# Performance work log

Measured on AMD Instinct MI355X. Metric: run time of the kernel, lower is better.

Reference implementation:

```python
import jax, jax.numpy as jnp
import numpy as np

B = 32768          # batch size (positions)
PIECES = 32        # max active features per position
NNZ = B * PIECES
FT_OUT = 512
NFEAT = 768        # 64 squares * 6 piece types * 2 colors


def setup_inputs() -> dict:
    key = jax.random.key(0)
    k1, k2, k3, k4, k5, k6 = jax.random.split(key, 6)
    rows = jnp.repeat(jnp.arange(B, dtype=jnp.int64), PIECES)  # batch index per nnz
    stm_cols = jax.random.randint(k1, (NNZ,), 0, NFEAT, dtype=jnp.int64)
    nstm_cols = jax.random.randint(k2, (NNZ,), 0, NFEAT, dtype=jnp.int64)
    stm_indices = jnp.stack([rows, stm_cols], axis=0)   # [2, NNZ]
    nstm_indices = jnp.stack([rows, nstm_cols], axis=0)  # [2, NNZ]
    values = jnp.ones((NNZ,), dtype=jnp.float32)
    ft_w = jax.random.normal(k3, (FT_OUT, NFEAT), dtype=jnp.float32) * 0.05
    ft_b = jax.random.normal(k4, (FT_OUT,), dtype=jnp.float32) * 0.05
    out_w = jax.random.normal(k5, (1, 2 * FT_OUT), dtype=jnp.float32) * 0.05
    out_b = jax.random.normal(k6, (1,), dtype=jnp.float32) * 0.05
    return {
        "stm_indices": stm_indices,
        "nstm_indices": nstm_indices,
        "values": values,
        "size": B,
        "ft_w": ft_w,
        "ft_b": ft_b,
        "out_w": out_w,
        "out_b": out_b,
    }


def reference(stm_indices, nstm_indices, values, size, ft_w, ft_b, out_w, out_b):
    # sparse_coo_tensor(...).to_dense(): scatter-add values into dense [size, 768]
    board_stm = jnp.zeros((size, NFEAT), dtype=values.dtype).at[
        stm_indices[0], stm_indices[1]].add(values)
    board_nstm = jnp.zeros((size, NFEAT), dtype=values.dtype).at[
        nstm_indices[0], nstm_indices[1]].add(values)
    # shared feature transformer Linear(768, ft_out)
    stm_ft = board_stm @ ft_w.T + ft_b    # [B, FT_OUT]
    nstm_ft = board_nstm @ ft_w.T + ft_b  # [B, FT_OUT]
    hidden = jnp.clip(jnp.concatenate([stm_ft, nstm_ft], axis=1), 0.0, 1.0)
    return jax.nn.sigmoid(hidden @ out_w.T + out_b)  # [B, 1]
```

## Files before the change

kernel.cpp:

```cpp
#include <hip/hip_runtime.h>

#define BATCH  32768
#define PIECES 32
#define NNZ    (BATCH * PIECES)
#define FT_OUT 512
#define NFEAT  768
#define WSCALE 400.0f

#define POS_PER_BLOCK 32
#define NTHREADS 512
#define NBLOCKS (BATCH / POS_PER_BLOCK)
#define ROW_PITCH 784
#define SIDE_BYTES (POS_PER_BLOCK * ROW_PITCH)
#define PACC_OFF (2 * SIDE_BYTES)
#define LDS_TOTAL (PACC_OFF + 128)
#define SC_PITCH 33

typedef int v4i  __attribute__((ext_vector_type(4)));
typedef int v16i __attribute__((ext_vector_type(16)));

__global__ __launch_bounds__(256) void pack_w_i8(
    const float* __restrict__ ft_w, unsigned char* __restrict__ bpk)
{
    int gid = blockIdx.x * 256 + threadIdx.x;
    int t   = gid / 1536;
    int rem = gid - t * 1536;
    int s   = rem >> 6;
    int l   = rem & 63;
    int g   = l >> 5, ln = l & 31;
    int n   = t * 32 + ln;
    const float* src = ft_w + n * NFEAT + s * 32 + g * 16;
    unsigned ud[4];
    #pragma unroll
    for (int d = 0; d < 4; ++d) {
        unsigned u = 0;
        #pragma unroll
        for (int b = 0; b < 4; ++b) {
            float q = rintf(src[4 * d + b] * WSCALE);
            q = fminf(fmaxf(q, -127.0f), 127.0f);
            u |= ((unsigned)(int)q & 0xffu) << (8 * b);
        }
        ud[d] = u;
    }
    *(uint4*)(bpk + gid * 16) = make_uint4(ud[0], ud[1], ud[2], ud[3]);
}

__global__ __launch_bounds__(NTHREADS, 4) void nn_mfma(
    const int*   __restrict__ stm_idx,
    const int*   __restrict__ nstm_idx,
    const float* __restrict__ values,
    const unsigned char* __restrict__ bpk,
    const float* __restrict__ ft_b,
    const float* __restrict__ out_w,
    const float* __restrict__ out_b,
    float*       __restrict__ out)
{
    extern __shared__ __align__(16) unsigned char lds[];
    unsigned* ldsw = (unsigned*)lds;
    float*    scf  = (float*)lds;
    float*    pacc = (float*)(lds + PACC_OFF);

    const int tid  = threadIdx.x;
    const int pos0 = blockIdx.x * POS_PER_BLOCK;

    int colv[4], vqv[4];
    #pragma unroll
    for (int it = 0; it < 4; ++it) {
        int i    = tid + it * NTHREADS;
        int side = i >> 10;
        int r    = i & 1023;
        int nnz  = pos0 * PIECES + r;
        colv[it] = side ? nstm_idx[NNZ + nnz] : stm_idx[NNZ + nnz];
        vqv[it]  = (int)rintf(values[nnz]);
    }

    for (int i = tid; i < LDS_TOTAL / 16; i += NTHREADS)
        ((uint4*)lds)[i] = make_uint4(0u, 0u, 0u, 0u);
    __syncthreads();

    #pragma unroll
    for (int it = 0; it < 4; ++it) {
        int i    = tid + it * NTHREADS;
        int side = i >> 10;
        int pos  = (i & 1023) >> 5;
        int dw   = (side * SIDE_BYTES + pos * ROW_PITCH) >> 2;
        atomicAdd(&ldsw[dw + (colv[it] >> 2)],
                  (unsigned)vqv[it] << (8 * (colv[it] & 3)));
    }
    __syncthreads();

    const int lane = tid & 63, wv = tid >> 6;
    const int ln = lane & 31, g = lane >> 5;
    const float inv_s = 1.0f / WSCALE;

    v16i acc[2][2];
    #pragma unroll
    for (int q = 0; q < 2; ++q)
        #pragma unroll
        for (int sd = 0; sd < 2; ++sd)
            #pragma unroll
            for (int e = 0; e < 16; ++e) acc[q][sd][e] = 0;

    const unsigned char* a0p = lds + ln * ROW_PITCH + g * 16;
    const unsigned char* a1p = a0p + SIDE_BYTES;
    const unsigned char* bp0 = bpk + ((wv * 2 + 0) * 24) * 1024 + lane * 16;
    const unsigned char* bp1 = bpk + ((wv * 2 + 1) * 24) * 1024 + lane * 16;

    #pragma unroll 4
    for (int ks = 0; ks < 24; ++ks) {
        uint4 aw0 = *(const uint4*)(a0p + ks * 32);
        uint4 aw1 = *(const uint4*)(a1p + ks * 32);
        uint4 bw0 = *(const uint4*)(bp0 + ks * 1024);
        uint4 bw1 = *(const uint4*)(bp1 + ks * 1024);
        v4i af0 = __builtin_bit_cast(v4i, aw0);
        v4i af1 = __builtin_bit_cast(v4i, aw1);
        v4i bf0 = __builtin_bit_cast(v4i, bw0);
        v4i bf1 = __builtin_bit_cast(v4i, bw1);
        acc[0][0] = __builtin_amdgcn_mfma_i32_32x32x32_i8(af0, bf0, acc[0][0], 0, 0, 0);
        acc[0][1] = __builtin_amdgcn_mfma_i32_32x32x32_i8(af1, bf0, acc[0][1], 0, 0, 0);
        acc[1][0] = __builtin_amdgcn_mfma_i32_32x32x32_i8(af0, bf1, acc[1][0], 0, 0, 0);
        acc[1][1] = __builtin_amdgcn_mfma_i32_32x32x32_i8(af1, bf1, acc[1][1], 0, 0, 0);
    }

    float pp[16];
    #pragma unroll
    for (int r = 0; r < 16; ++r) pp[r] = 0.f;

    #pragma unroll
    for (int q = 0; q < 2; ++q) {
        int   n    = (wv * 2 + q) * 32 + ln;
        float bias = ft_b[n];
        float ow0  = out_w[n];
        float ow1  = out_w[FT_OUT + n];
        #pragma unroll
        for (int r = 0; r < 16; ++r) {
            float h0 = fminf(fmaxf((float)acc[q][0][r] * inv_s + bias, 0.f), 1.f);
            float h1 = fminf(fmaxf((float)acc[q][1][r] * inv_s + bias, 0.f), 1.f);
            pp[r] += h0 * ow0 + h1 * ow1;
        }
    }

    __syncthreads();
    {
        int base = wv * (32 * SC_PITCH) + ln * SC_PITCH;
        #pragma unroll
        for (int r = 0; r < 16; ++r) {
            int m = (r & 3) + 8 * (r >> 2) + 4 * g;
            scf[base + m] = pp[r];
        }
    }
    __syncthreads();
    {
        int m = tid & 31, j = tid >> 5;
        float s = 0.f;
        #pragma unroll
        for (int i = 0; i < 16; ++i) {
            int p   = i * 16 + j;
            int wvp = p >> 5, lnp = p & 31;
            s += scf[wvp * (32 * SC_PITCH) + lnp * SC_PITCH + m];
        }
        atomicAdd(&pacc[m], s);
    }
    __syncthreads();

    if (tid < POS_PER_BLOCK) {
        float p = pacc[tid] + out_b[0];
        out[pos0 + tid] = 1.0f / (1.0f + expf(-p));
    }
}

extern "C" void kernel_launch(void* const* d_in, const int* in_sizes, int n_in,
                              void* d_out, int out_size, void* d_ws, size_t ws_size,
                              hipStream_t stream)
{
    const int*   stm    = (const int*)  d_in[0];
    const int*   nstm   = (const int*)  d_in[1];
    const float* values = (const float*)d_in[2];
    const float* ft_w   = (const float*)d_in[4];
    const float* ft_b   = (const float*)d_in[5];
    const float* out_w  = (const float*)d_in[6];
    const float* out_b  = (const float*)d_in[7];

    unsigned char* bpk = (unsigned char*)d_ws;

    (void)hipFuncSetAttribute((const void*)nn_mfma,
                              hipFuncAttributeMaxDynamicSharedMemorySize,
                              LDS_TOTAL);

    pack_w_i8<<<dim3(96), dim3(256), 0, stream>>>(ft_w, bpk);
    nn_mfma<<<dim3(NBLOCKS), dim3(NTHREADS), LDS_TOTAL, stream>>>(
        stm, nstm, values, bpk, ft_b, out_w, out_b, (float*)d_out);
}
```

Measured before the change: 105.1 us.

## Double positions per block to reuse packed weight fragments across more MFMAs

Each block now handles 64 positions instead of 32, so every weight fragment loaded from global memory feeds four MFMAs instead of two, halving total weight traffic. The epilogue reduction runs in two phases, one per 32-position half, reusing the same scratch area in LDS. In exchange LDS per block roughly doubles, accumulator registers double, occupancy hint drops from 4 to 2 blocks per CU, and the grid has half as many blocks.

```diff
diff --git a/kernel.cpp b/kernel.cpp
--- a/kernel.cpp
+++ b/kernel.cpp
@@ -7,13 +7,13 @@
 #define NFEAT  768
 #define WSCALE 400.0f
 
-#define POS_PER_BLOCK 32
+#define POS_PER_BLOCK 64
 #define NTHREADS 512
 #define NBLOCKS (BATCH / POS_PER_BLOCK)
 #define ROW_PITCH 784
 #define SIDE_BYTES (POS_PER_BLOCK * ROW_PITCH)
 #define PACC_OFF (2 * SIDE_BYTES)
-#define LDS_TOTAL (PACC_OFF + 128)
+#define LDS_TOTAL (PACC_OFF + 256)
 #define SC_PITCH 33
 
 typedef int v4i  __attribute__((ext_vector_type(4)));
@@ -45,7 +45,7 @@
     *(uint4*)(bpk + gid * 16) = make_uint4(ud[0], ud[1], ud[2], ud[3]);
 }
 
-__global__ __launch_bounds__(NTHREADS, 4) void nn_mfma(
+__global__ __launch_bounds__(NTHREADS, 2) void nn_mfma(
     const int*   __restrict__ stm_idx,
     const int*   __restrict__ nstm_idx,
     const float* __restrict__ values,
@@ -63,12 +63,12 @@
     const int tid  = threadIdx.x;
     const int pos0 = blockIdx.x * POS_PER_BLOCK;
 
-    int colv[4], vqv[4];
-    #pragma unroll
-    for (int it = 0; it < 4; ++it) {
+    int colv[8], vqv[8];
+    #pragma unroll
+    for (int it = 0; it < 8; ++it) {
         int i    = tid + it * NTHREADS;
-        int side = i >> 10;
-        int r    = i & 1023;
+        int side = i >> 11;
+        int r    = i & 2047;
         int nnz  = pos0 * PIECES + r;
         colv[it] = side ? nstm_idx[NNZ + nnz] : stm_idx[NNZ + nnz];
         vqv[it]  = (int)rintf(values[nnz]);
@@ -79,10 +79,10 @@
     __syncthreads();
 
     #pragma unroll
-    for (int it = 0; it < 4; ++it) {
+    for (int it = 0; it < 8; ++it) {
         int i    = tid + it * NTHREADS;
-        int side = i >> 10;
-        int pos  = (i & 1023) >> 5;
+        int side = i >> 11;
+        int pos  = (i & 2047) >> 5;
         int dw   = (side * SIDE_BYTES + pos * ROW_PITCH) >> 2;
         atomicAdd(&ldsw[dw + (colv[it] >> 2)],
                   (unsigned)vqv[it] << (8 * (colv[it] & 3)));
@@ -93,75 +93,87 @@
     const int ln = lane & 31, g = lane >> 5;
     const float inv_s = 1.0f / WSCALE;
 
-    v16i acc[2][2];
+    v16i acc[2][4];
     #pragma unroll
     for (int q = 0; q < 2; ++q)
         #pragma unroll
-        for (int sd = 0; sd < 2; ++sd)
+        for (int mt = 0; mt < 4; ++mt)
             #pragma unroll
-            for (int e = 0; e < 16; ++e) acc[q][sd][e] = 0;
-
-    const unsigned char* a0p = lds + ln * ROW_PITCH + g * 16;
-    const unsigned char* a1p = a0p + SIDE_BYTES;
+            for (int e = 0; e < 16; ++e) acc[q][mt][e] = 0;
+
+    const unsigned char* ap[4];
+    #pragma unroll
+    for (int mt = 0; mt < 4; ++mt)
+        ap[mt] = lds + (mt >> 1) * SIDE_BYTES
+               + (((mt & 1) * 32) + ln) * ROW_PITCH + g * 16;
     const unsigned char* bp0 = bpk + ((wv * 2 + 0) * 24) * 1024 + lane * 16;
     const unsigned char* bp1 = bpk + ((wv * 2 + 1) * 24) * 1024 + lane * 16;
 
-    #pragma unroll 4
+    #pragma unroll 2
     for (int ks = 0; ks < 24; ++ks) {
-        uint4 aw0 = *(const uint4*)(a0p + ks * 32);
-        uint4 aw1 = *(const uint4*)(a1p + ks * 32);
         uint4 bw0 = *(const uint4*)(bp0 + ks * 1024);
         uint4 bw1 = *(const uint4*)(bp1 + ks * 1024);
+        uint4 aw0 = *(const uint4*)(ap[0] + ks * 32);
+        uint4 aw1 = *(const uint4*)(ap[1] + ks * 32);
+        uint4 aw2 = *(const uint4*)(ap[2] + ks * 32);
+        uint4 aw3 = *(const uint4*)(ap[3] + ks * 32);
+        v4i bf0 = __builtin_bit_cast(v4i, bw0);
+        v4i bf1 = __builtin_bit_cast(v4i, bw1);
         v4i af0 = __builtin_bit_cast(v4i, aw0);
         v4i af1 = __builtin_bit_cast(v4i, aw1);
-        v4i bf0 = __builtin_bit_cast(v4i, bw0);
-        v4i bf1 = __builtin_bit_cast(v4i, bw1);
+        v4i af2 = __builtin_bit_cast(v4i, aw2);
+        v4i af3 = __builtin_bit_cast(v4i, aw3);
         acc[0][0] = __builtin_amdgcn_mfma_i32_32x32x32_i8(af0, bf0, acc[0][0], 0, 0, 0);
         acc[0][1] = __builtin_amdgcn_mfma_i32_32x32x32_i8(af1, bf0, acc[0][1], 0, 0, 0);
+        acc[0][2] = __builtin_amdgcn_mfma_i32_32x32x32_i8(af2, bf0, acc[0][2], 0, 0, 0);
+        acc[0][3] = __builtin_amdgcn_mfma_i32_32x32x32_i8(af3, bf0, acc[0][3], 0, 0, 0);
         acc[1][0] = __builtin_amdgcn_mfma_i32_32x32x32_i8(af0, bf1, acc[1][0], 0, 0, 0);
         acc[1][1] = __builtin_amdgcn_mfma_i32_32x32x32_i8(af1, bf1, acc[1][1], 0, 0, 0);
-    }
-
-    float pp[16];
-    #pragma unroll
-    for (int r = 0; r < 16; ++r) pp[r] = 0.f;
-
-    #pragma unroll
-    for (int q = 0; q < 2; ++q) {
-        int   n    = (wv * 2 + q) * 32 + ln;
-        float bias = ft_b[n];
-        float ow0  = out_w[n];
-        float ow1  = out_w[FT_OUT + n];
+        acc[1][2] = __builtin_amdgcn_mfma_i32_32x32x32_i8(af2, bf1, acc[1][2], 0, 0, 0);
+        acc[1][3] = __builtin_amdgcn_mfma_i32_32x32x32_i8(af3, bf1, acc[1][3], 0, 0, 0);
+    }
+
+    const int   n0   = (wv * 2 + 0) * 32 + ln;
+    const int   n1   = (wv * 2 + 1) * 32 + ln;
+    const float b0   = ft_b[n0],          b1   = ft_b[n1];
+    const float ow00 = out_w[n0],         ow01 = out_w[n1];
+    const float ow10 = out_w[FT_OUT + n0], ow11 = out_w[FT_OUT + n1];
+
+    __syncthreads();
+
+    #pragma unroll
+    for (int ph = 0; ph < 2; ++ph) {
+        float pp[16];
         #pragma unroll
         for (int r = 0; r < 16; ++r) {
-            float h0 = fminf(fmaxf((float)acc[q][0][r] * inv_s + bias, 0.f), 1.f);
-            float h1 = fminf(fmaxf((float)acc[q][1][r] * inv_s + bias, 0.f), 1.f);
-            pp[r] += h0 * ow0 + h1 * ow1;
-        }
-    }
-
-    __syncthreads();
-    {
-        int base = wv * (32 * SC_PITCH) + ln * SC_PITCH;
-        #pragma unroll
-        for (int r = 0; r < 16; ++r) {
-            int m = (r & 3) + 8 * (r >> 2) + 4 * g;
-            scf[base + m] = pp[r];
-        }
-    }
-    __syncthreads();
-    {
-        int m = tid & 31, j = tid >> 5;
-        float s = 0.f;
-        #pragma unroll
-        for (int i = 0; i < 16; ++i) {
-            int p   = i * 16 + j;
-            int wvp = p >> 5, lnp = p & 31;
-            s += scf[wvp * (32 * SC_PITCH) + lnp * SC_PITCH + m];
-        }
-        atomicAdd(&pacc[m], s);
-    }
-    __syncthreads();
+            float h00 = fminf(fmaxf((float)acc[0][ph][r]     * inv_s + b0, 0.f), 1.f);
+            float h01 = fminf(fmaxf((float)acc[1][ph][r]     * inv_s + b1, 0.f), 1.f);
+            float h10 = fminf(fmaxf((float)acc[0][ph + 2][r] * inv_s + b0, 0.f), 1.f);
+            float h11 = fminf(fmaxf((float)acc[1][ph + 2][r] * inv_s + b1, 0.f), 1.f);
+            pp[r] = h00 * ow00 + h01 * ow01 + h10 * ow10 + h11 * ow11;
+        }
+        {
+            int base = wv * (32 * SC_PITCH) + ln * SC_PITCH;
+            #pragma unroll
+            for (int r = 0; r < 16; ++r) {
+                int m = (r & 3) + 8 * (r >> 2) + 4 * g;
+                scf[base + m] = pp[r];
+            }
+        }
+        __syncthreads();
+        {
+            int m = tid & 31, j = tid >> 5;
+            float s = 0.f;
+            #pragma unroll
+            for (int i = 0; i < 16; ++i) {
+                int p   = i * 16 + j;
+                int wvp = p >> 5, lnp = p & 31;
+                s += scf[wvp * (32 * SC_PITCH) + lnp * SC_PITCH + m];
+            }
+            atomicAdd(&pacc[ph * 32 + m], s);
+        }
+        __syncthreads();
+    }
 
     if (tid < POS_PER_BLOCK) {
         float p = pacc[tid] + out_b[0];
```

New measurement: 106.5 us. Within noise of the previous version (+1.3%).

## Process four position groups per block with double-buffered LDS scatter prefetch

Applied to the files above, without the earlier changes.

Each block now handles four groups of 32 positions instead of one. While the MFMA loop runs on the current group, it loads the next group's sparse indices and scatters them into a second LDS buffer. Bias and output-weight loads are hoisted out of the loop, and the occupancy hint drops from 4 to 2 blocks per CU. The aim is to hide index-load and scatter latency inside each block, at the cost of a quarter as many blocks, twice the LDS per block and less cross-block latency hiding.

```diff
diff --git a/kernel.cpp b/kernel.cpp
--- a/kernel.cpp
+++ b/kernel.cpp
@@ -7,12 +7,15 @@
 #define NFEAT  768
 #define WSCALE 400.0f
 
-#define POS_PER_BLOCK 32
+#define POS_PER_GROUP 32
+#define GROUPS 4
+#define POS_PER_BLOCK (POS_PER_GROUP * GROUPS)
 #define NTHREADS 512
 #define NBLOCKS (BATCH / POS_PER_BLOCK)
 #define ROW_PITCH 784
-#define SIDE_BYTES (POS_PER_BLOCK * ROW_PITCH)
-#define PACC_OFF (2 * SIDE_BYTES)
+#define SIDE_BYTES (POS_PER_GROUP * ROW_PITCH)
+#define BUF_BYTES (2 * SIDE_BYTES)
+#define PACC_OFF (2 * BUF_BYTES)
 #define LDS_TOTAL (PACC_OFF + 128)
 #define SC_PITCH 33
 
@@ -45,7 +48,7 @@
     *(uint4*)(bpk + gid * 16) = make_uint4(ud[0], ud[1], ud[2], ud[3]);
 }
 
-__global__ __launch_bounds__(NTHREADS, 4) void nn_mfma(
+__global__ __launch_bounds__(NTHREADS, 2) void nn_mfma(
     const int*   __restrict__ stm_idx,
     const int*   __restrict__ nstm_idx,
     const float* __restrict__ values,
@@ -57,11 +60,21 @@
 {
     extern __shared__ __align__(16) unsigned char lds[];
     unsigned* ldsw = (unsigned*)lds;
-    float*    scf  = (float*)lds;
     float*    pacc = (float*)(lds + PACC_OFF);
 
     const int tid  = threadIdx.x;
-    const int pos0 = blockIdx.x * POS_PER_BLOCK;
+    const int lane = tid & 63, wv = tid >> 6;
+    const int ln = lane & 31, g2 = lane >> 5;
+    const float inv_s = 1.0f / WSCALE;
+    const int pos_base = blockIdx.x * POS_PER_BLOCK;
+
+    const int   n0   = (wv * 2 + 0) * 32 + ln;
+    const int   n1   = (wv * 2 + 1) * 32 + ln;
+    const float b0   = ft_b[n0],           b1   = ft_b[n1];
+    const float ow00 = out_w[n0],          ow01 = out_w[n1];
+    const float ow10 = out_w[FT_OUT + n0], ow11 = out_w[FT_OUT + n1];
+    const unsigned char* bp0 = bpk + ((wv * 2 + 0) * 24) * 1024 + lane * 16;
+    const unsigned char* bp1 = bpk + ((wv * 2 + 1) * 24) * 1024 + lane * 16;
 
     int colv[4], vqv[4];
     #pragma unroll
@@ -69,15 +82,13 @@
         int i    = tid + it * NTHREADS;
         int side = i >> 10;
         int r    = i & 1023;
-        int nnz  = pos0 * PIECES + r;
+        int nnz  = pos_base * PIECES + r;
         colv[it] = side ? nstm_idx[NNZ + nnz] : stm_idx[NNZ + nnz];
         vqv[it]  = (int)rintf(values[nnz]);
     }
-
     for (int i = tid; i < LDS_TOTAL / 16; i += NTHREADS)
         ((uint4*)lds)[i] = make_uint4(0u, 0u, 0u, 0u);
     __syncthreads();
-
     #pragma unroll
     for (int it = 0; it < 4; ++it) {
         int i    = tid + it * NTHREADS;
@@ -89,83 +100,107 @@
     }
     __syncthreads();
 
-    const int lane = tid & 63, wv = tid >> 6;
-    const int ln = lane & 31, g = lane >> 5;
-    const float inv_s = 1.0f / WSCALE;
-
-    v16i acc[2][2];
-    #pragma unroll
-    for (int q = 0; q < 2; ++q)
+    for (int grp = 0; grp < GROUPS; ++grp) {
+        const int cur = grp & 1;
+        unsigned char* buf  = lds + cur * BUF_BYTES;
+        unsigned char* nbuf = lds + (1 - cur) * BUF_BYTES;
+        const unsigned nbuf_dw = (unsigned)((1 - cur) * BUF_BYTES) >> 2;
+
+        int ncol[4], nvq[4];
+        if (grp + 1 < GROUPS) {
+            #pragma unroll
+            for (int it = 0; it < 4; ++it) {
+                int i    = tid + it * NTHREADS;
+                int side = i >> 10;
+                int r    = i & 1023;
+                int nnz  = (pos_base + (grp + 1) * POS_PER_GROUP) * PIECES + r;
+                ncol[it] = side ? nstm_idx[NNZ + nnz] : stm_idx[NNZ + nnz];
+                nvq[it]  = (int)rintf(values[nnz]);
+            }
+        }
+
+        v16i acc[2][2];
         #pragma unroll
-        for (int sd = 0; sd < 2; ++sd)
-            #pragma unroll
-            for (int e = 0; e < 16; ++e) acc[q][sd][e] = 0;
-
-    const unsigned char* a0p = lds + ln * ROW_PITCH + g * 16;
-    const unsigned char* a1p = a0p + SIDE_BYTES;
-    const unsigned char* bp0 = bpk + ((wv * 2 + 0) * 24) * 1024 + lane * 16;
-    const unsigned char* bp1 = bpk + ((wv * 2 + 1) * 24) * 1024 + lane * 16;
-
-    #pragma unroll 4
-    for (int ks = 0; ks < 24; ++ks) {
-        uint4 aw0 = *(const uint4*)(a0p + ks * 32);
-        uint4 aw1 = *(const uint4*)(a1p + ks * 32);
-        uint4 bw0 = *(const uint4*)(bp0 + ks * 1024);
-        uint4 bw1 = *(const uint4*)(bp1 + ks * 1024);
-        v4i af0 = __builtin_bit_cast(v4i, aw0);
-        v4i af1 = __builtin_bit_cast(v4i, aw1);
-        v4i bf0 = __builtin_bit_cast(v4i, bw0);
-        v4i bf1 = __builtin_bit_cast(v4i, bw1);
-        acc[0][0] = __builtin_amdgcn_mfma_i32_32x32x32_i8(af0, bf0, acc[0][0], 0, 0, 0);
-        acc[0][1] = __builtin_amdgcn_mfma_i32_32x32x32_i8(af1, bf0, acc[0][1], 0, 0, 0);
-        acc[1][0] = __builtin_amdgcn_mfma_i32_32x32x32_i8(af0, bf1, acc[1][0], 0, 0, 0);
-        acc[1][1] = __builtin_amdgcn_mfma_i32_32x32x32_i8(af1, bf1, acc[1][1], 0, 0, 0);
-    }
-
-    float pp[16];
-    #pragma unroll
-    for (int r = 0; r < 16; ++r) pp[r] = 0.f;
-
-    #pragma unroll
-    for (int q = 0; q < 2; ++q) {
-        int   n    = (wv * 2 + q) * 32 + ln;
-        float bias = ft_b[n];
-        float ow0  = out_w[n];
-        float ow1  = out_w[FT_OUT + n];
+        for (int q = 0; q < 2; ++q)
+            #pragma unroll
+            for (int sd = 0; sd < 2; ++sd)
+                #pragma unroll
+                for (int e = 0; e < 16; ++e) acc[q][sd][e] = 0;
+
+        const unsigned char* a0p = buf + ln * ROW_PITCH + g2 * 16;
+        const unsigned char* a1p = a0p + SIDE_BYTES;
+
+        #pragma unroll 4
+        for (int ks = 0; ks < 24; ++ks) {
+            uint4 aw0 = *(const uint4*)(a0p + ks * 32);
+            uint4 aw1 = *(const uint4*)(a1p + ks * 32);
+            uint4 bw0 = *(const uint4*)(bp0 + ks * 1024);
+            uint4 bw1 = *(const uint4*)(bp1 + ks * 1024);
+            v4i af0 = __builtin_bit_cast(v4i, aw0);
+            v4i af1 = __builtin_bit_cast(v4i, aw1);
+            v4i bf0 = __builtin_bit_cast(v4i, bw0);
+            v4i bf1 = __builtin_bit_cast(v4i, bw1);
+            acc[0][0] = __builtin_amdgcn_mfma_i32_32x32x32_i8(af0, bf0, acc[0][0], 0, 0, 0);
+            acc[0][1] = __builtin_amdgcn_mfma_i32_32x32x32_i8(af1, bf0, acc[0][1], 0, 0, 0);
+            acc[1][0] = __builtin_amdgcn_mfma_i32_32x32x32_i8(af0, bf1, acc[1][0], 0, 0, 0);
+            acc[1][1] = __builtin_amdgcn_mfma_i32_32x32x32_i8(af1, bf1, acc[1][1], 0, 0, 0);
+        }
+
+        float pp[16];
         #pragma unroll
         for (int r = 0; r < 16; ++r) {
-            float h0 = fminf(fmaxf((float)acc[q][0][r] * inv_s + bias, 0.f), 1.f);
-            float h1 = fminf(fmaxf((float)acc[q][1][r] * inv_s + bias, 0.f), 1.f);
-            pp[r] += h0 * ow0 + h1 * ow1;
-        }
-    }
-
-    __syncthreads();
-    {
-        int base = wv * (32 * SC_PITCH) + ln * SC_PITCH;
-        #pragma unroll
-        for (int r = 0; r < 16; ++r) {
-            int m = (r & 3) + 8 * (r >> 2) + 4 * g;
-            scf[base + m] = pp[r];
-        }
-    }
-    __syncthreads();
-    {
-        int m = tid & 31, j = tid >> 5;
-        float s = 0.f;
-        #pragma unroll
-        for (int i = 0; i < 16; ++i) {
-            int p   = i * 16 + j;
-            int wvp = p >> 5, lnp = p & 31;
-            s += scf[wvp * (32 * SC_PITCH) + lnp * SC_PITCH + m];
-        }
-        atomicAdd(&pacc[m], s);
-    }
-    __syncthreads();
-
-    if (tid < POS_PER_BLOCK) {
-        float p = pacc[tid] + out_b[0];
-        out[pos0 + tid] = 1.0f / (1.0f + expf(-p));
+            float h00 = fminf(fmaxf((float)acc[0][0][r] * inv_s + b0, 0.f), 1.f);
+            float h01 = fminf(fmaxf((float)acc[1][0][r] * inv_s + b1, 0.f), 1.f);
+            float h10 = fminf(fmaxf((float)acc[0][1][r] * inv_s + b0, 0.f), 1.f);
+            float h11 = fminf(fmaxf((float)acc[1][1][r] * inv_s + b1, 0.f), 1.f);
+            pp[r] = h00 * ow00 + h01 * ow01 + h10 * ow10 + h11 * ow11;
+        }
+
+        if (grp + 1 < GROUPS) {
+            #pragma unroll
+            for (int it = 0; it < 4; ++it) {
+                int i    = tid + it * NTHREADS;
+                int side = i >> 10;
+                int pos  = (i & 1023) >> 5;
+                int dw   = nbuf_dw + ((side * SIDE_BYTES + pos * ROW_PITCH) >> 2);
+                atomicAdd(&ldsw[dw + (ncol[it] >> 2)],
+                          (unsigned)nvq[it] << (8 * (ncol[it] & 3)));
+            }
+        }
+        __syncthreads();
+
+        float* scf = (float*)buf;
+        {
+            int base = wv * (32 * SC_PITCH) + ln * SC_PITCH;
+            #pragma unroll
+            for (int r = 0; r < 16; ++r) {
+                int m = (r & 3) + 8 * (r >> 2) + 4 * g2;
+                scf[base + m] = pp[r];
+            }
+        }
+        __syncthreads();
+        {
+            int m = tid & 31, j = tid >> 5;
+            float s = 0.f;
+            #pragma unroll
+            for (int i = 0; i < 16; ++i) {
+                int p = i * 16 + j;
+                s += scf[(p >> 5) * (32 * SC_PITCH) + (p & 31) * SC_PITCH + m];
+            }
+            atomicAdd(&pacc[m], s);
+        }
+        __syncthreads();
+
+        if (tid < POS_PER_GROUP) {
+            float p = pacc[tid] + out_b[0];
+            out[pos_base + grp * POS_PER_GROUP + tid] = 1.0f / (1.0f + expf(-p));
+            pacc[tid] = 0.0f;
+        }
+        if (grp + 2 <= GROUPS) {
+            for (int i = tid; i < BUF_BYTES / 16; i += NTHREADS)
+                ((uint4*)buf)[i] = make_uint4(0u, 0u, 0u, 0u);
+        }
+        __syncthreads();
     }
 }
 
```

New measurement: 121.2 us. +15.3%, slower.
